# Kernel optimization log

Hardware: AMD Instinct MI355X
Metric: run time of the kernel (lower is better)

## Reference

```python
import jax, jax.numpy as jnp
import numpy as np

B, S, D = 2, 1024, 1024
NH, DQK, DH = 8, 64, 128
CAP = 15.0
EPS = 1e-6


def setup_inputs() -> dict:
    key = jax.random.key(0)
    ks = jax.random.split(key, 8)
    s = 0.02
    return {
        "x": jax.random.normal(ks[0], (B, S, D), jnp.float32),
        "Wq": jax.random.normal(ks[1], (D, NH * DQK), jnp.float32) * s,
        "Wk": jax.random.normal(ks[2], (D, NH * DQK), jnp.float32) * s,
        "Wv": jax.random.normal(ks[3], (D, NH * DH), jnp.float32) * s,
        "Wi": jax.random.normal(ks[4], (D, NH), jnp.float32) * s,
        "bi": jnp.zeros((NH,), jnp.float32),
        "Wf": jax.random.normal(ks[5], (D, NH), jnp.float32) * s,
        "bf": jnp.ones((NH,), jnp.float32),
        "Wog": jax.random.normal(ks[6], (D, D), jnp.float32) * s,
        "ln_w": jnp.ones((NH, DH), jnp.float32),
        "ln_b": jnp.zeros((NH, DH), jnp.float32),
        "Wout": jax.random.normal(ks[7], (NH * DH, D), jnp.float32) * s,
    }


def _mlstm_scan(q, k, v, i, f):
    # q,k: [S,B,NH,DQK]; v: [S,B,NH,DH]; i,f: [S,B,NH]
    b, nh, dqk, dh = q.shape[1], q.shape[2], q.shape[3], v.shape[3]
    scale = dqk ** -0.5
    c0 = jnp.zeros((b, nh, dqk, dh), jnp.float32)
    m0 = jnp.zeros((b, nh), jnp.float32)

    def step(carry, inp):
        c, m = carry
        qt, kt, vt, it, ft = inp
        flog = jax.nn.log_sigmoid(ft)
        m_new = jnp.maximum(flog + m, it)
        f_act = jnp.exp(flog + m - m_new)
        i_act = jnp.exp(it - m_new)
        kv = jnp.einsum('bhi,bhj->bhij', kt, vt)
        c_new = f_act[..., None, None] * c + i_act[..., None, None] * kv
        ht = jnp.einsum('bhij,bhi->bhj', c_new, qt * scale)
        return (c_new, m_new), ht

    _, h = jax.lax.scan(step, (c0, m0), (q, k, v, i, f))
    return h  # [S,B,NH,DH]


def reference(x, Wq, Wk, Wv, Wi, bi, Wf, bf, Wog, ln_w, ln_b, Wout):
    b, s, d = x.shape
    nh, dh = ln_w.shape
    dqk = Wq.shape[1] // nh
    # projections -> time-major [S,B,NH,*]
    q = (x @ Wq).reshape(b, s, nh, dqk).transpose(1, 0, 2, 3)
    k = (x @ Wk).reshape(b, s, nh, dqk).transpose(1, 0, 2, 3)
    v = (x @ Wv).reshape(b, s, nh, dh).transpose(1, 0, 2, 3)
    i = (x @ Wi + bi).transpose(1, 0, 2)
    f = (x @ Wf + bf).transpose(1, 0, 2)
    h = _mlstm_scan(q, k, v, i, f)           # [S,B,NH,DH]
    h = h.transpose(1, 2, 0, 3)              # [B,NH,S,DH]
    # per-head layernorm (unbiased=False variance)
    mean = h.mean(-1, keepdims=True)
    var = ((h - mean) ** 2).mean(-1, keepdims=True)
    hn = (h - mean) / jnp.sqrt(var + EPS)
    hn = hn * ln_w[None, :, None, :] + ln_b[None, :, None, :]
    hn = hn.transpose(0, 2, 1, 3).reshape(b, s, nh * dh)  # [B,S,v_dim]
    o = jax.nn.sigmoid(jnp.tanh((x @ Wog) / CAP) * CAP)
    return (hn * o) @ Wout
```

## Files before the change

### kernel.cpp

```cpp
#include <hip/hip_runtime.h>
#include <math.h>

#define NB_B   2
#define NB_S   1024
#define NB_D   1024
#define NB_NH  8
#define NB_DQK 64
#define NB_DH  128
#define NCH    8
#define CL     128

typedef __attribute__((ext_vector_type(8))) short  short8v;
typedef __attribute__((ext_vector_type(4))) float  f32x4;
typedef __attribute__((ext_vector_type(8))) unsigned short ushort8v;
typedef __attribute__((ext_vector_type(4))) unsigned short ushort4v;

__device__ __forceinline__ unsigned short f2bf(float f) {
  unsigned u = __float_as_uint(f);
  unsigned r = (u + 0x7FFFu + ((u >> 16) & 1u)) >> 16;
  return (unsigned short)r;
}
__device__ __forceinline__ float bf2f(unsigned short h) {
  return __uint_as_float(((unsigned)h) << 16);
}

#define GLD_LDS16(g, l) __builtin_amdgcn_global_load_lds( \
    (const __attribute__((address_space(1))) void*)(g),   \
    (__attribute__((address_space(3))) void*)(l), 16, 0, 0)

#define MFMA_BF16(a, b, c) __builtin_amdgcn_mfma_f32_16x16x32_bf16((a), (b), (c), 0, 0, 0)

constexpr size_t BF(size_t elems) { return elems / 2; }
constexpr size_t SZ_PQK = 2048ull * 1024;
constexpr size_t SZ_PVX = BF(2048ull * 2048);
constexpr size_t SZ_XH  = BF(2048ull * 1024);
constexpr size_t SZ_XL  = BF(2048ull * 1024);
constexpr size_t SZ_WHI = BF(3072ull * 1024);
constexpr size_t SZ_WLO = BF(1024ull * 1024);
constexpr size_t SZ_WTO = BF(1024ull * 1024);
constexpr size_t SZ_GBUF= 16ull * 1024;
constexpr size_t SZ_DL  = 16ull * 8 * 8192;
constexpr size_t SZ_CB  = 16ull * 8 * 8192;
constexpr size_t SZ_HNG = BF(2048ull * 1024);

constexpr size_t OFF_PQK = 0;
constexpr size_t OFF_PVX = OFF_PQK + SZ_PQK;
constexpr size_t OFF_XH  = OFF_PVX + SZ_PVX;
constexpr size_t OFF_XL  = OFF_XH  + SZ_XH;
constexpr size_t OFF_WHI = OFF_XL  + SZ_XL;
constexpr size_t OFF_WLO = OFF_WHI + SZ_WHI;
constexpr size_t OFF_WTO = OFF_WLO + SZ_WLO;
constexpr size_t OFF_IV  = OFF_WTO + SZ_WTO;
constexpr size_t OFF_FV  = OFF_IV  + SZ_GBUF;
constexpr size_t OFF_G   = OFF_FV  + SZ_GBUF;
constexpr size_t OFF_GM  = OFF_G   + SZ_GBUF;
constexpr size_t OFF_DL  = OFF_GM  + SZ_GBUF;
constexpr size_t OFF_CB  = OFF_DL  + SZ_DL;
constexpr size_t OFF_HNG = OFF_CB  + SZ_CB;
constexpr size_t WS_TOTAL = OFF_HNG + SZ_HNG;
static_assert(OFF_XH == OFF_PVX + 2097152, "Pvx is 2048x2048 bf16 = 2,097,152 float slots");

__global__ __launch_bounds__(64) void row_pre(
    const float* __restrict__ x,
    const float* __restrict__ Wi, const float* __restrict__ bi,
    const float* __restrict__ Wf, const float* __restrict__ bf,
    unsigned short* __restrict__ xh, unsigned short* __restrict__ xl,
    float* __restrict__ iv, float* __restrict__ fv)
{
  const int row = blockIdx.x, l = threadIdx.x;
  const float4* xr4 = (const float4*)(x + (size_t)row * NB_D);
  float ai[8] = {}, af[8] = {};
  #pragma unroll
  for (int p = 0; p < 4; ++p) {
    int q4i = l + p * 64;
    float4 xv = xr4[q4i];
    int k0 = q4i * 4;
    const float* xs = (const float*)&xv;
    ushort4v h4, l4;
    #pragma unroll
    for (int j = 0; j < 4; ++j) {
      float xsv = xs[j];
      unsigned short hh = f2bf(xsv);
      h4[j] = hh; l4[j] = f2bf(xsv - bf2f(hh));
      const float4* wi4 = (const float4*)(Wi + (size_t)(k0 + j) * 8);
      const float4* wf4 = (const float4*)(Wf + (size_t)(k0 + j) * 8);
      float4 w0 = wi4[0], w1 = wi4[1];
      float4 v0 = wf4[0], v1 = wf4[1];
      ai[0] += xsv*w0.x; ai[1] += xsv*w0.y; ai[2] += xsv*w0.z; ai[3] += xsv*w0.w;
      ai[4] += xsv*w1.x; ai[5] += xsv*w1.y; ai[6] += xsv*w1.z; ai[7] += xsv*w1.w;
      af[0] += xsv*v0.x; af[1] += xsv*v0.y; af[2] += xsv*v0.z; af[3] += xsv*v0.w;
      af[4] += xsv*v1.x; af[5] += xsv*v1.y; af[6] += xsv*v1.z; af[7] += xsv*v1.w;
    }
    *(ushort4v*)(xh + (size_t)row * NB_D + k0) = h4;
    *(ushort4v*)(xl + (size_t)row * NB_D + k0) = l4;
  }
  #pragma unroll
  for (int off = 1; off < 64; off <<= 1) {
    #pragma unroll
    for (int cc = 0; cc < 8; ++cc) {
      ai[cc] += __shfl_xor(ai[cc], off);
      af[cc] += __shfl_xor(af[cc], off);
    }
  }
  if (l == 0) {
    int b = row >> 10, s = row & (NB_S - 1);
    #pragma unroll
    for (int cc = 0; cc < 8; ++cc) {
      iv[(size_t)(b*NB_NH + cc) * NB_S + s] = ai[cc] + bi[cc];
      fv[(size_t)(b*NB_NH + cc) * NB_S + s] = af[cc] + bf[cc];
    }
  }
}

__device__ __forceinline__ void transp_body(
    const float* __restrict__ src,
    unsigned short* __restrict__ hi, unsigned short* __restrict__ lo,
    int N, int nt, int kt, int tid, float (*Ls)[65])
{
  #pragma unroll
  for (int p = 0; p < 16; ++p) {
    int lin = p * 256 + tid;
    int kr = lin >> 6, nc = lin & 63;
    Ls[kr][nc] = src[(size_t)(kt*64 + kr) * N + nt*64 + nc];
  }
  __syncthreads();
  #pragma unroll
  for (int p = 0; p < 16; ++p) {
    int lin = p * 256 + tid;
    int nr = lin >> 6, kc = lin & 63;
    float v = Ls[kc][nr];
    unsigned short h = f2bf(v);
    size_t di = (size_t)(nt*64 + nr) * 1024 + kt*64 + kc;
    hi[di] = h;
    if (lo) lo[di] = f2bf(v - bf2f(h));
  }
}

__global__ __launch_bounds__(256) void transp5(
    const float* __restrict__ Wq, const float* __restrict__ Wk,
    const float* __restrict__ Wv, const float* __restrict__ Wog,
    const float* __restrict__ Wout,
    unsigned short* __restrict__ Whi, unsigned short* __restrict__ Wlo,
    unsigned short* __restrict__ WtO)
{
  __shared__ float Ls[64][65];
  const int x = blockIdx.x, kt = blockIdx.y, tid = threadIdx.x;
  if (x < 8)       transp_body(Wq,   Whi,              Wlo,            512,  x,      kt, tid, Ls);
  else if (x < 16) transp_body(Wk,   Whi +  512*1024,  Wlo + 512*1024, 512,  x - 8,  kt, tid, Ls);
  else if (x < 32) transp_body(Wv,   Whi + 1024*1024,  nullptr,        1024, x - 16, kt, tid, Ls);
  else if (x < 48) transp_body(Wog,  Whi + 2048*1024,  nullptr,        1024, x - 32, kt, tid, Ls);
  else             transp_body(Wout, WtO,              nullptr,        1024, x - 48, kt, tid, Ls);
}

__global__ __launch_bounds__(256) void gemm_proj(
    const unsigned short* __restrict__ xh,
    const unsigned short* __restrict__ xl,
    const unsigned short* __restrict__ Whi,
    const unsigned short* __restrict__ Wlo,
    float* __restrict__ Pqk, unsigned short* __restrict__ Pvx)
{
  __shared__ __align__(16) char smem[49152];
  const int tid  = threadIdx.x;
  const int bid  = ((blockIdx.x & 7) << 6) | (blockIdx.x >> 3);
  const int wid  = tid >> 6, lane = tid & 63;
  const int wm   = wid >> 1, wn = wid & 1;
  const int lrow = lane & 15;
  const int lk   = (lane >> 4) * 16;
  const int srow = tid >> 3;
  const int scb  = (tid & 7) << 4;
  const int ldsW = wid * 1024;

  if (!(bid & 1)) {
    const int h  = bid >> 1;
    const int ct = h & 7, bm = h >> 3;
    char* Ah = smem;
    char* Al = smem + 8192;
    char* Bh = smem + 16384;
    char* Bl = smem + 32768;
    const char* xhB = (const char*)xh;
    const char* xlB = (const char*)xl;
    const char* whB = (const char*)(Whi + (size_t)ct*128*1024);
    const char* wlB = (const char*)(Wlo + (size_t)ct*128*1024);

    size_t gA[2], gB[4];
    #pragma unroll
    for (int i = 0; i < 2; ++i) {
      int row = i * 32 + srow;
      int cbs = scb ^ ((row & 7) << 4);
      gA[i] = (size_t)(bm*64 + row) * 2048 + cbs;
    }
    #pragma unroll
    for (int i = 0; i < 4; ++i) {
      int row = i * 32 + srow;
      int cbs = scb ^ ((row & 7) << 4);
      gB[i] = (size_t)row * 2048 + cbs;
    }

    f32x4 acc[2][4];
    const f32x4 z4 = { 0.f, 0.f, 0.f, 0.f };
    #pragma unroll
    for (int m = 0; m < 2; ++m)
      #pragma unroll
      for (int n = 0; n < 4; ++n) acc[m][n] = z4;

    for (int kt = 0; kt < 16; ++kt) {
      __syncthreads();
      #pragma unroll
      for (int i = 0; i < 2; ++i) GLD_LDS16(xhB + gA[i] + kt*128, Ah + i*4096 + ldsW);
      #pragma unroll
      for (int i = 0; i < 2; ++i) GLD_LDS16(xlB + gA[i] + kt*128, Al + i*4096 + ldsW);
      #pragma unroll
      for (int i = 0; i < 4; ++i) GLD_LDS16(whB + gB[i] + kt*128, Bh + i*4096 + ldsW);
      #pragma unroll
      for (int i = 0; i < 4; ++i) GLD_LDS16(wlB + gB[i] + kt*128, Bl + i*4096 + ldsW);
      __syncthreads();

      #pragma unroll
      for (int kk = 0; kk < 2; ++kk) {
        short8v ah[2], al[2], bh[4], bl[4];
        #pragma unroll
        for (int m = 0; m < 2; ++m) {
          int row = wm*32 + m*16 + lrow;
          int kb  = (kk*64 + lk) ^ ((row & 7) << 4);
          ah[m] = *(const short8v*)(Ah + row*128 + kb);
          al[m] = *(const short8v*)(Al + row*128 + kb);
        }
        #pragma unroll
        for (int n = 0; n < 4; ++n) {
          int row = wn*64 + n*16 + lrow;
          int kb  = (kk*64 + lk) ^ ((row & 7) << 4);
          bh[n] = *(const short8v*)(Bh + row*128 + kb);
          bl[n] = *(const short8v*)(Bl + row*128 + kb);
        }
        #pragma unroll
        for (int m = 0; m < 2; ++m)
          #pragma unroll
          for (int n = 0; n < 4; ++n) {
            acc[m][n] = MFMA_BF16(ah[m], bh[n], acc[m][n]);
            acc[m][n] = MFMA_BF16(al[m], bh[n], acc[m][n]);
            acc[m][n] = MFMA_BF16(ah[m], bl[n], acc[m][n]);
          }
      }
    }

    const int crow0 = bm*64 + wm*32 + ((lane >> 4) << 2);
    const int ccol0 = ct*128 + wn*64 + lrow;
    #pragma unroll
    for (int m = 0; m < 2; ++m)
      #pragma unroll
      for (int n = 0; n < 4; ++n)
        #pragma unroll
        for (int r = 0; r < 4; ++r)
          Pqk[(size_t)(crow0 + m*16 + r) * 1024 + ccol0 + n*16] = acc[m][n][r];
  } else {
    const int l  = bid >> 1;
    const int ct = l & 15, bm = l >> 4;
    char* As = smem;
    char* Bs = smem + 16384;
    const char* xhB = (const char*)xh;
    const char* wB  = (const char*)(Whi + (size_t)(8 + ct)*128*1024);

    size_t gA[4], gB[4];
    #pragma unroll
    for (int i = 0; i < 4; ++i) {
      int row = i * 32 + srow;
      int cbs = scb ^ ((row & 7) << 4);
      gA[i] = (size_t)(bm*128 + row) * 2048 + cbs;
      gB[i] = (size_t)row * 2048 + cbs;
    }

    f32x4 acc[4][4];
    const f32x4 z4 = { 0.f, 0.f, 0.f, 0.f };
    #pragma unroll
    for (int m = 0; m < 4; ++m)
      #pragma unroll
      for (int n = 0; n < 4; ++n) acc[m][n] = z4;

    for (int kt = 0; kt < 16; ++kt) {
      __syncthreads();
      #pragma unroll
      for (int i = 0; i < 4; ++i) GLD_LDS16(xhB + gA[i] + kt*128, As + i*4096 + ldsW);
      #pragma unroll
      for (int i = 0; i < 4; ++i) GLD_LDS16(wB  + gB[i] + kt*128, Bs + i*4096 + ldsW);
      __syncthreads();

      #pragma unroll
      for (int kk = 0; kk < 2; ++kk) {
        short8v a[4], b[4];
        #pragma unroll
        for (int m = 0; m < 4; ++m) {
          int row = wm*64 + m*16 + lrow;
          int kb  = (kk*64 + lk) ^ ((row & 7) << 4);
          a[m] = *(const short8v*)(As + row*128 + kb);
        }
        #pragma unroll
        for (int n = 0; n < 4; ++n) {
          int row = wn*64 + n*16 + lrow;
          int kb  = (kk*64 + lk) ^ ((row & 7) << 4);
          b[n] = *(const short8v*)(Bs + row*128 + kb);
        }
        #pragma unroll
        for (int m = 0; m < 4; ++m)
          #pragma unroll
          for (int n = 0; n < 4; ++n)
            acc[m][n] = MFMA_BF16(a[m], b[n], acc[m][n]);
      }
    }

    const int crow0 = bm*128 + wm*64 + ((lane >> 4) << 2);
    const int ccol0 = ct*128 + wn*64 + lrow;
    #pragma unroll
    for (int m = 0; m < 4; ++m)
      #pragma unroll
      for (int n = 0; n < 4; ++n)
        #pragma unroll
        for (int r = 0; r < 4; ++r)
          Pvx[(size_t)(crow0 + m*16 + r) * 2048 + ccol0 + n*16] = f2bf(acc[m][n][r]);
  }
}

__global__ __launch_bounds__(256) void gemm_out64(
    const unsigned short* __restrict__ A,
    const unsigned short* __restrict__ Bt,
    float* __restrict__ C, int ldc)
{
  __shared__ __align__(16) unsigned short As[128*64];
  __shared__ __align__(16) unsigned short Bs[64*64];
  const int tid  = threadIdx.x;
  const int bid  = ((blockIdx.x & 7) << 5) | (blockIdx.x >> 3);
  const int cn   = bid & 15, bm = bid >> 4;
  const int wid  = tid >> 6, lane = tid & 63;
  const int wm   = wid >> 1, wn = wid & 1;
  const int lrow = lane & 15;
  const int lk   = (lane >> 4) * 16;

  f32x4 acc[4][2];
  const f32x4 z4 = { 0.f, 0.f, 0.f, 0.f };
  #pragma unroll
  for (int m = 0; m < 4; ++m)
    #pragma unroll
    for (int n = 0; n < 2; ++n) acc[m][n] = z4;

  const int srow = tid >> 3;
  const int scb  = (tid & 7) << 4;
  const char* Ab = (const char*)A;
  const char* Bb = (const char*)Bt;
  size_t gA[4], gB[2];
  #pragma unroll
  for (int i = 0; i < 4; ++i) {
    int row = i * 32 + srow;
    int cbs = scb ^ ((row & 7) << 4);
    gA[i] = (size_t)(bm*128 + row) * 2048 + cbs;
  }
  #pragma unroll
  for (int i = 0; i < 2; ++i) {
    int row = i * 32 + srow;
    int cbs = scb ^ ((row & 7) << 4);
    gB[i] = (size_t)(cn*64 + row) * 2048 + cbs;
  }
  const int ldsW = wid * 1024;

  for (int kt = 0; kt < 16; ++kt) {
    __syncthreads();
    #pragma unroll
    for (int i = 0; i < 4; ++i)
      GLD_LDS16(Ab + gA[i] + kt*128, (char*)As + i*4096 + ldsW);
    #pragma unroll
    for (int i = 0; i < 2; ++i)
      GLD_LDS16(Bb + gB[i] + kt*128, (char*)Bs + i*4096 + ldsW);
    __syncthreads();

    #pragma unroll
    for (int kk = 0; kk < 2; ++kk) {
      short8v a[4], b[2];
      #pragma unroll
      for (int m = 0; m < 4; ++m) {
        int row = wm*64 + m*16 + lrow;
        int kb  = (kk*64 + lk) ^ ((row & 7) << 4);
        a[m] = *(const short8v*)((const char*)As + row*128 + kb);
      }
      #pragma unroll
      for (int n = 0; n < 2; ++n) {
        int row = wn*32 + n*16 + lrow;
        int kb  = (kk*64 + lk) ^ ((row & 7) << 4);
        b[n] = *(const short8v*)((const char*)Bs + row*128 + kb);
      }
      #pragma unroll
      for (int m = 0; m < 4; ++m)
        #pragma unroll
        for (int n = 0; n < 2; ++n)
          acc[m][n] = MFMA_BF16(a[m], b[n], acc[m][n]);
    }
  }

  const int crow0 = bm*128 + wm*64 + ((lane >> 4) << 2);
  const int ccol0 = cn*64 + wn*32 + (lane & 15);
  #pragma unroll
  for (int m = 0; m < 4; ++m)
    #pragma unroll
    for (int n = 0; n < 2; ++n)
      #pragma unroll
      for (int r = 0; r < 4; ++r)
        C[(size_t)(crow0 + m*16 + r) * ldc + ccol0 + n*16] = acc[m][n][r];
}

__global__ __launch_bounds__(64) void gate_scan(
    const float* __restrict__ iv, const float* __restrict__ fv,
    float* __restrict__ gv, float* __restrict__ Gv)
{
  const int bh = blockIdx.x, l = threadIdx.x;
  const int base = bh * NB_S + l * 16;
  float fl[16];
  float run = 0.f;
  #pragma unroll
  for (int u = 0; u < 16; ++u) {
    float fr = fv[base + u];
    float flog = (fr >= 0.f) ? -log1pf(expf(-fr)) : (fr - log1pf(expf(fr)));
    run += flog; fl[u] = run;
  }
  float tot = run, sc = tot;
  #pragma unroll
  for (int off = 1; off < 64; off <<= 1) {
    float t = __shfl_up(sc, off);
    if (l >= off) sc += t;
  }
  float excl = sc - tot;
  float gm[16]; float rmax = -1e30f;
  #pragma unroll
  for (int u = 0; u < 16; ++u) {
    float bt = excl + fl[u];
    float g = iv[base + u] - bt;
    gv[base + u] = g;
    rmax = fmaxf(rmax, g); gm[u] = rmax;
  }
  float mx = rmax;
  #pragma unroll
  for (int off = 1; off < 64; off <<= 1) {
    float t = __shfl_up(mx, off);
    if (l >= off) mx = fmaxf(mx, t);
  }
  float em = __shfl_up(mx, 1);
  if (l == 0) em = -1e30f;
  #pragma unroll
  for (int u = 0; u < 16; ++u)
    Gv[base + u] = fmaxf(0.f, fmaxf(em, gm[u]));
}

__global__ __launch_bounds__(128) void chunk_local(
    const float* __restrict__ Pqk, const unsigned short* __restrict__ Pvx,
    const float* __restrict__ gv, const float* __restrict__ Gv,
    float* __restrict__ Dloc)
{
  __shared__ float ks[16][68];
  __shared__ float vs[16][132];
  __shared__ float wsg[16];
  const int bx = blockIdx.x, bh = bx >> 3, c = bx & 7;
  const int b = bh >> 3, h = bh & 7;
  const int tid = threadIdx.x;
  const int rg = tid >> 3, cg = tid & 7;
  const int i0 = rg * 4;
  float acc[4][16] = {};
  const float Gend = Gv[bh*NB_S + c*CL + CL - 1];
  const float* kbp = Pqk + ((size_t)b*NB_S + c*CL) * 1024 + 512 + h*NB_DQK;
  const unsigned short* vbp = Pvx + ((size_t)b*NB_S + c*CL) * 2048 + h*NB_DH;
  const float* gbp = gv + bh*NB_S + c*CL;
  for (int sb = 0; sb < 8; ++sb) {
    __syncthreads();
    #pragma unroll
    for (int p = 0; p < 2; ++p) {
      int qd = tid + p*128; int r = qd >> 4, cq = qd & 15;
      *(float4*)(&ks[r][cq*4]) = *(const float4*)(kbp + (size_t)(sb*16 + r)*1024 + cq*4);
    }
    #pragma unroll
    for (int p = 0; p < 4; ++p) {
      int qd = tid + p*128; int r = qd >> 5, cq = qd & 31;
      ushort4v v4 = *(const ushort4v*)(vbp + (size_t)(sb*16 + r)*2048 + cq*4);
      vs[r][cq*4+0] = bf2f(v4[0]); vs[r][cq*4+1] = bf2f(v4[1]);
      vs[r][cq*4+2] = bf2f(v4[2]); vs[r][cq*4+3] = bf2f(v4[3]);
    }
    if (tid < 16) wsg[tid] = expf(gbp[sb*16 + tid] - Gend);
    __syncthreads();
    #pragma unroll
    for (int s = 0; s < 16; ++s) {
      float w = wsg[s];
      float4 kq = *(const float4*)(&ks[s][i0]);
      float wk[4] = { w*kq.x, w*kq.y, w*kq.z, w*kq.w };
      #pragma unroll
      for (int m = 0; m < 4; ++m) {
        float4 vq = *(const float4*)(&vs[s][cg*4 + m*32]);
        #pragma unroll
        for (int u = 0; u < 4; ++u) {
          acc[u][m*4+0] += wk[u]*vq.x;
          acc[u][m*4+1] += wk[u]*vq.y;
          acc[u][m*4+2] += wk[u]*vq.z;
          acc[u][m*4+3] += wk[u]*vq.w;
        }
      }
    }
  }
  float* dst = Dloc + ((size_t)bh*NCH + c) * (NB_DQK*NB_DH);
  #pragma unroll
  for (int u = 0; u < 4; ++u)
    #pragma unroll
    for (int m = 0; m < 4; ++m) {
      float4 o4 = { acc[u][m*4+0], acc[u][m*4+1], acc[u][m*4+2], acc[u][m*4+3] };
      *(float4*)(dst + (size_t)(i0+u)*NB_DH + cg*4 + m*32) = o4;
    }
}

__global__ __launch_bounds__(256) void chunk_combine(
    const float* __restrict__ Dloc, const float* __restrict__ Gv,
    float* __restrict__ Cbef)
{
  const int bh = blockIdx.x >> 3, sl = blockIdx.x & 7;
  const int fo = sl*1024 + threadIdx.x*4;
  float4 acc = { 0.f, 0.f, 0.f, 0.f };
  float Gprev = 0.f;
  for (int c = 0; c < NCH; ++c) {
    const float* dl = Dloc + ((size_t)bh*NCH + c)*8192 + fo;
    float* cb = Cbef + ((size_t)bh*NCH + c)*8192 + fo;
    float Gend = Gv[bh*NB_S + c*CL + CL - 1];
    float decay = (c == 0) ? 0.f : expf(Gprev - Gend);
    *(float4*)cb = acc;
    float4 d = *(const float4*)dl;
    acc.x = acc.x*decay + d.x;
    acc.y = acc.y*decay + d.y;
    acc.z = acc.z*decay + d.z;
    acc.w = acc.w*decay + d.w;
    Gprev = Gend;
  }
}

__global__ __launch_bounds__(256,1) void chunk_out(
    const float* __restrict__ Pqk, const unsigned short* __restrict__ Pvx,
    const float* __restrict__ gv, const float* __restrict__ Gv,
    const float* __restrict__ Cbef,
    const float* __restrict__ lnw, const float* __restrict__ lnb,
    unsigned short* __restrict__ hng)
{
  __shared__ __align__(16) char smem[131072];
  __shared__ float gsh[128], Gsh[128], rsh[128];
  constexpr int QH = 0, QL = 8192, KH = 16384, KL = 32768;
  constexpr int ATT = 49152, VT = 65536, CBH = 98304, CBL = 114688;

  const int bx = ((blockIdx.x & 7) << 5) | (blockIdx.x >> 3);
  const int half = bx & 1, c = (bx >> 1) & 7, bh = bx >> 4;
  const int b = bh >> 3, h = bh & 7;
  const int tid = threadIdx.x;
  const int wid = tid >> 6, lane = tid & 63;
  const int lrow = lane & 15;
  const int lkB  = (lane >> 4) * 16;
  const size_t rowbase = (size_t)b*NB_S + (size_t)c*CL;
  const int sgbase = bh*NB_S + c*CL;

  if (tid < 128) {
    float gval = gv[sgbase + tid];
    float Gval = Gv[sgbase + tid];
    gsh[tid] = gval; Gsh[tid] = Gval;
    float Gprev = (c > 0) ? Gv[sgbase - 1] : 0.f;
    rsh[tid] = 0.125f * expf(Gprev - Gval);
  }

  #pragma unroll
  for (int p = 0; p < 4; ++p) {
    int lin = p*256 + tid;
    int row = lin >> 4, i0 = (lin & 15) * 4;
    float4 v4 = *(const float4*)(Pqk + (rowbase + half*64 + row)*1024 + h*NB_DQK + i0);
    float vv[4] = { v4.x, v4.y, v4.z, v4.w };
    ushort4v h4, l4;
    #pragma unroll
    for (int j = 0; j < 4; ++j) {
      unsigned short hh = f2bf(vv[j]); h4[j] = hh; l4[j] = f2bf(vv[j] - bf2f(hh));
    }
    int off = (row*128 + i0*2) ^ ((row & 7) << 4);
    *(ushort4v*)(smem + QH + off) = h4;
    *(ushort4v*)(smem + QL + off) = l4;
  }
  #pragma unroll
  for (int p = 0; p < 8; ++p) {
    int lin = p*256 + tid;
    int row = lin >> 4, i0 = (lin & 15) * 4;
    float4 v4 = *(const float4*)(Pqk + (rowbase + row)*1024 + 512 + h*NB_DQK + i0);
    float vv[4] = { v4.x, v4.y, v4.z, v4.w };
    ushort4v h4, l4;
    #pragma unroll
    for (int j = 0; j < 4; ++j) {
      unsigned short hh = f2bf(vv[j]); h4[j] = hh; l4[j] = f2bf(vv[j] - bf2f(hh));
    }
    int off = (row*128 + i0*2) ^ ((row & 7) << 4);
    *(ushort4v*)(smem + KH + off) = h4;
    *(ushort4v*)(smem + KL + off) = l4;
  }
  #pragma unroll
  for (int p = 0; p < 8; ++p) {
    int lin = p*256 + tid;
    int s = lin >> 4, j0 = (lin & 15) * 8;
    ushort8v v8 = *(const ushort8v*)(Pvx + (rowbase + s)*2048 + h*NB_DH + j0);
    #pragma unroll
    for (int j = 0; j < 8; ++j) {
      int jj = j0 + j;
      int off = (jj*256 + s*2) ^ ((jj & 7) << 4);
      *(unsigned short*)(smem + VT + off) = v8[j];
    }
  }
  {
    const float* Cbp = Cbef + ((size_t)bh*NCH + c)*(NB_DQK*NB_DH);
    #pragma unroll
    for (int p = 0; p < 8; ++p) {
      int lin = p*256 + tid;
      int i = lin >> 5, j0 = (lin & 31) * 4;
      float4 v4 = *(const float4*)(Cbp + (size_t)i*NB_DH + j0);
      float vv[4] = { v4.x, v4.y, v4.z, v4.w };
      #pragma unroll
      for (int w = 0; w < 4; ++w) {
        int jj = j0 + w;
        int off = (jj*128 + i*2) ^ ((jj & 7) << 4);
        unsigned short hh = f2bf(vv[w]);
        *(unsigned short*)(smem + CBH + off) = hh;
        *(unsigned short*)(smem + CBL + off) = f2bf(vv[w] - bf2f(hh));
      }
    }
  }
  __syncthreads();

  const f32x4 z4 = { 0.f, 0.f, 0.f, 0.f };
  const int trow = wid*16 + lrow;

  f32x4 sacc[8];
  #pragma unroll
  for (int n = 0; n < 8; ++n) sacc[n] = z4;
  #pragma unroll
  for (int kk = 0; kk < 2; ++kk) {
    int qb = kk*64 + lkB;
    int ab = (trow*128 + qb) ^ ((trow & 7) << 4);
    short8v aqh = *(const short8v*)(smem + QH + ab);
    short8v aql = *(const short8v*)(smem + QL + ab);
    #pragma unroll
    for (int n = 0; n < 8; ++n) {
      int srw = n*16 + lrow;
      int bb = (srw*128 + qb) ^ ((srw & 7) << 4);
      short8v bkh = *(const short8v*)(smem + KH + bb);
      short8v bkl = *(const short8v*)(smem + KL + bb);
      sacc[n] = MFMA_BF16(aqh, bkh, sacc[n]);
      sacc[n] = MFMA_BF16(aql, bkh, sacc[n]);
      sacc[n] = MFMA_BF16(aqh, bkl, sacc[n]);
    }
  }
  {
    int td[4]; float gt[4];
    #pragma unroll
    for (int r = 0; r < 4; ++r) {
      td[r] = wid*16 + ((lane >> 4) << 2) + r;
      gt[r] = Gsh[half*64 + td[r]];
    }
    #pragma unroll
    for (int n = 0; n < 8; ++n) {
      int s = n*16 + lrow;
      float gs = gsh[s];
      #pragma unroll
      for (int r = 0; r < 4; ++r) {
        float w = 0.125f * expf(gs - gt[r]);
        float val = (s <= half*64 + td[r]) ? sacc[n][r]*w : 0.f;
        int off = (td[r]*256 + s*2) ^ ((td[r] & 7) << 4);
        *(unsigned short*)(smem + ATT + off) = f2bf(val);
      }
    }
  }

  f32x4 h2[8];
  #pragma unroll
  for (int n = 0; n < 8; ++n) h2[n] = z4;
  #pragma unroll
  for (int kk = 0; kk < 2; ++kk) {
    int qb = kk*64 + lkB;
    int ab = (trow*128 + qb) ^ ((trow & 7) << 4);
    short8v aqh = *(const short8v*)(smem + QH + ab);
    short8v aql = *(const short8v*)(smem + QL + ab);
    #pragma unroll
    for (int n = 0; n < 8; ++n) {
      int jrw = n*16 + lrow;
      int bb = (jrw*128 + qb) ^ ((jrw & 7) << 4);
      short8v bch = *(const short8v*)(smem + CBH + bb);
      short8v bcl = *(const short8v*)(smem + CBL + bb);
      h2[n] = MFMA_BF16(aqh, bch, h2[n]);
      h2[n] = MFMA_BF16(aql, bch, h2[n]);
      h2[n] = MFMA_BF16(aqh, bcl, h2[n]);
    }
  }
  __syncthreads();

  f32x4 h1[8];
  #pragma unroll
  for (int n = 0; n < 8; ++n) h1[n] = z4;
  #pragma unroll
  for (int kk = 0; kk < 4; ++kk) {
    int ab = (trow*256 + kk*64 + lkB) ^ ((trow & 7) << 4);
    short8v aat = *(const short8v*)(smem + ATT + ab);
    #pragma unroll
    for (int n = 0; n < 8; ++n) {
      int jrw = n*16 + lrow;
      int bb = (jrw*256 + kk*64 + lkB) ^ ((jrw & 7) << 4);
      short8v bvt = *(const short8v*)(smem + VT + bb);
      h1[n] = MFMA_BF16(aat, bvt, h1[n]);
    }
  }
  __syncthreads();

  float* Hb = (float*)smem;
  {
    #pragma unroll
    for (int r = 0; r < 4; ++r) {
      int tl = wid*16 + ((lane >> 4) << 2) + r;
      float rr = rsh[half*64 + tl];
      #pragma unroll
      for (int n = 0; n < 8; ++n)
        Hb[tl*132 + n*16 + lrow] = h1[n][r] + rr*h2[n][r];
    }
  }
  __syncthreads();

  const int tr = tid >> 4, tc = tid & 15;
  float lw[8], lb[8];
  {
    float4 a0 = *(const float4*)(lnw + h*NB_DH + tc*4);
    float4 a1 = *(const float4*)(lnw + h*NB_DH + tc*4 + 64);
    lw[0]=a0.x; lw[1]=a0.y; lw[2]=a0.z; lw[3]=a0.w;
    lw[4]=a1.x; lw[5]=a1.y; lw[6]=a1.z; lw[7]=a1.w;
    float4 b0 = *(const float4*)(lnb + h*NB_DH + tc*4);
    float4 b1 = *(const float4*)(lnb + h*NB_DH + tc*4 + 64);
    lb[0]=b0.x; lb[1]=b0.y; lb[2]=b0.z; lb[3]=b0.w;
    lb[4]=b1.x; lb[5]=b1.y; lb[6]=b1.z; lb[7]=b1.w;
  }
  #pragma unroll
  for (int u = 0; u < 4; ++u) {
    int tl = tr*4 + u;
    int t  = half*64 + tl;
    float hrow[8];
    float4 hl0 = *(const float4*)(&Hb[tl*132 + tc*4]);
    float4 hl1 = *(const float4*)(&Hb[tl*132 + tc*4 + 64]);
    hrow[0]=hl0.x; hrow[1]=hl0.y; hrow[2]=hl0.z; hrow[3]=hl0.w;
    hrow[4]=hl1.x; hrow[5]=hl1.y; hrow[6]=hl1.z; hrow[7]=hl1.w;
    float sum = 0.f, ssq = 0.f;
    #pragma unroll
    for (int x = 0; x < 8; ++x) { sum += hrow[x]; ssq += hrow[x]*hrow[x]; }
    #pragma unroll
    for (int off = 1; off < 16; off <<= 1) {
      sum += __shfl_xor(sum, off);
      ssq += __shfl_xor(ssq, off);
    }
    float mean = sum * (1.f/NB_DH);
    float var  = ssq * (1.f/NB_DH) - mean*mean;
    float rstd = rsqrtf(var + 1e-6f);
    #pragma unroll
    for (int m = 0; m < 2; ++m) {
      ushort4v xo4 = *(const ushort4v*)(Pvx + (rowbase + t)*2048 + 1024 + h*NB_DH + tc*4 + m*64);
      float xov[4] = { bf2f(xo4[0]), bf2f(xo4[1]), bf2f(xo4[2]), bf2f(xo4[3]) };
      unsigned short res[4];
      #pragma unroll
      for (int w = 0; w < 4; ++w) {
        int x = m*4 + w;
        float hn = (hrow[x] - mean)*rstd*lw[x] + lb[x];
        float tt = tanhf(xov[w]*(1.f/15.f))*15.f;
        float o = 1.f/(1.f + expf(-tt));
        res[w] = f2bf(hn*o);
      }
      ushort4v r4 = { res[0], res[1], res[2], res[3] };
      *(ushort4v*)(hng + (rowbase + t)*1024 + h*NB_DH + tc*4 + m*64) = r4;
    }
  }
}

extern "C" void kernel_launch(void* const* d_in, const int* in_sizes, int n_in,
                              void* d_out, int out_size, void* d_ws, size_t ws_size,
                              hipStream_t stream)
{
  (void)in_sizes; (void)n_in; (void)out_size; (void)ws_size;
  const float* x   = (const float*)d_in[0];
  const float* Wq  = (const float*)d_in[1];
  const float* Wk  = (const float*)d_in[2];
  const float* Wv  = (const float*)d_in[3];
  const float* Wi  = (const float*)d_in[4];
  const float* bi  = (const float*)d_in[5];
  const float* Wf  = (const float*)d_in[6];
  const float* bf  = (const float*)d_in[7];
  const float* Wog = (const float*)d_in[8];
  const float* lnw = (const float*)d_in[9];
  const float* lnb = (const float*)d_in[10];
  const float* Wout= (const float*)d_in[11];
  float* out = (float*)d_out;
  float* ws  = (float*)d_ws;

  float*          Pqk = ws + OFF_PQK;
  unsigned short* Pvx = (unsigned short*)(ws + OFF_PVX);
  unsigned short* xh  = (unsigned short*)(ws + OFF_XH);
  unsigned short* xl  = (unsigned short*)(ws + OFF_XL);
  unsigned short* Whi = (unsigned short*)(ws + OFF_WHI);
  unsigned short* Wlo = (unsigned short*)(ws + OFF_WLO);
  unsigned short* WtO = (unsigned short*)(ws + OFF_WTO);
  float*          iv  = ws + OFF_IV;
  float*          fv  = ws + OFF_FV;
  float*          g   = ws + OFF_G;
  float*          G   = ws + OFF_GM;
  float*          Dl  = ws + OFF_DL;
  float*          Cb  = ws + OFF_CB;
  unsigned short* hng = (unsigned short*)(ws + OFF_HNG);

  row_pre <<<2048, 64, 0, stream>>>(x, Wi, bi, Wf, bf, xh, xl, iv, fv);
  transp5 <<<dim3(64,16), 256, 0, stream>>>(Wq, Wk, Wv, Wog, Wout, Whi, Wlo, WtO);
  gate_scan<<<16, 64, 0, stream>>>(iv, fv, g, G);

  gemm_proj<<<512, 256, 0, stream>>>(xh, xl, Whi, Wlo, Pqk, Pvx);

  chunk_local  <<<128, 128, 0, stream>>>(Pqk, Pvx, g, G, Dl);
  chunk_combine<<<128, 256, 0, stream>>>(Dl, G, Cb);
  chunk_out    <<<256, 256, 0, stream>>>(Pqk, Pvx, g, G, Cb, lnw, lnb, hng);

  gemm_out64<<<256, 256, 0, stream>>>(hng, WtO, out, 1024);
}
```

Before: 135.1 us.

## Fuse row_pre with weight transpose and fold chunk_combine into chunk_out

Merges the per-row x split/gate projection kernel and the weight transpose kernel into one prep launch, packing 4 rows per 256-thread block. Removes chunk_combine and its Cbef buffer: each chunk_out block now recomputes its inter-chunk state as an exp-weighted sum of all earlier chunks' local states read from Dloc. This saves two launches and one global round trip, but adds redundant reads and FMAs that grow with chunk index (up to 7 chunks of 32KB per block).

Result: faster. 129.6 us (-4.0%).

```diff
diff --git a/kernel.cpp b/kernel.cpp
--- a/kernel.cpp
+++ b/kernel.cpp
@@ -40,7 +40,6 @@
 constexpr size_t SZ_WTO = BF(1024ull * 1024);
 constexpr size_t SZ_GBUF= 16ull * 1024;
 constexpr size_t SZ_DL  = 16ull * 8 * 8192;
-constexpr size_t SZ_CB  = 16ull * 8 * 8192;
 constexpr size_t SZ_HNG = BF(2048ull * 1024);
 
 constexpr size_t OFF_PQK = 0;
@@ -55,62 +54,9 @@
 constexpr size_t OFF_G   = OFF_FV  + SZ_GBUF;
 constexpr size_t OFF_GM  = OFF_G   + SZ_GBUF;
 constexpr size_t OFF_DL  = OFF_GM  + SZ_GBUF;
-constexpr size_t OFF_CB  = OFF_DL  + SZ_DL;
-constexpr size_t OFF_HNG = OFF_CB  + SZ_CB;
+constexpr size_t OFF_HNG = OFF_DL  + SZ_DL;
 constexpr size_t WS_TOTAL = OFF_HNG + SZ_HNG;
 static_assert(OFF_XH == OFF_PVX + 2097152, "Pvx is 2048x2048 bf16 = 2,097,152 float slots");
-
-__global__ __launch_bounds__(64) void row_pre(
-    const float* __restrict__ x,
-    const float* __restrict__ Wi, const float* __restrict__ bi,
-    const float* __restrict__ Wf, const float* __restrict__ bf,
-    unsigned short* __restrict__ xh, unsigned short* __restrict__ xl,
-    float* __restrict__ iv, float* __restrict__ fv)
-{
-  const int row = blockIdx.x, l = threadIdx.x;
-  const float4* xr4 = (const float4*)(x + (size_t)row * NB_D);
-  float ai[8] = {}, af[8] = {};
-  #pragma unroll
-  for (int p = 0; p < 4; ++p) {
-    int q4i = l + p * 64;
-    float4 xv = xr4[q4i];
-    int k0 = q4i * 4;
-    const float* xs = (const float*)&xv;
-    ushort4v h4, l4;
-    #pragma unroll
-    for (int j = 0; j < 4; ++j) {
-      float xsv = xs[j];
-      unsigned short hh = f2bf(xsv);
-      h4[j] = hh; l4[j] = f2bf(xsv - bf2f(hh));
-      const float4* wi4 = (const float4*)(Wi + (size_t)(k0 + j) * 8);
-      const float4* wf4 = (const float4*)(Wf + (size_t)(k0 + j) * 8);
-      float4 w0 = wi4[0], w1 = wi4[1];
-      float4 v0 = wf4[0], v1 = wf4[1];
-      ai[0] += xsv*w0.x; ai[1] += xsv*w0.y; ai[2] += xsv*w0.z; ai[3] += xsv*w0.w;
-      ai[4] += xsv*w1.x; ai[5] += xsv*w1.y; ai[6] += xsv*w1.z; ai[7] += xsv*w1.w;
-      af[0] += xsv*v0.x; af[1] += xsv*v0.y; af[2] += xsv*v0.z; af[3] += xsv*v0.w;
-      af[4] += xsv*v1.x; af[5] += xsv*v1.y; af[6] += xsv*v1.z; af[7] += xsv*v1.w;
-    }
-    *(ushort4v*)(xh + (size_t)row * NB_D + k0) = h4;
-    *(ushort4v*)(xl + (size_t)row * NB_D + k0) = l4;
-  }
-  #pragma unroll
-  for (int off = 1; off < 64; off <<= 1) {
-    #pragma unroll
-    for (int cc = 0; cc < 8; ++cc) {
-      ai[cc] += __shfl_xor(ai[cc], off);
-      af[cc] += __shfl_xor(af[cc], off);
-    }
-  }
-  if (l == 0) {
-    int b = row >> 10, s = row & (NB_S - 1);
-    #pragma unroll
-    for (int cc = 0; cc < 8; ++cc) {
-      iv[(size_t)(b*NB_NH + cc) * NB_S + s] = ai[cc] + bi[cc];
-      fv[(size_t)(b*NB_NH + cc) * NB_S + s] = af[cc] + bf[cc];
-    }
-  }
-}
 
 __device__ __forceinline__ void transp_body(
     const float* __restrict__ src,
@@ -136,20 +82,74 @@
   }
 }
 
-__global__ __launch_bounds__(256) void transp5(
+__global__ __launch_bounds__(256) void prep(
+    const float* __restrict__ x,
+    const float* __restrict__ Wi, const float* __restrict__ bi,
+    const float* __restrict__ Wf, const float* __restrict__ bf,
     const float* __restrict__ Wq, const float* __restrict__ Wk,
     const float* __restrict__ Wv, const float* __restrict__ Wog,
     const float* __restrict__ Wout,
+    unsigned short* __restrict__ xh, unsigned short* __restrict__ xl,
+    float* __restrict__ iv, float* __restrict__ fv,
     unsigned short* __restrict__ Whi, unsigned short* __restrict__ Wlo,
     unsigned short* __restrict__ WtO)
 {
   __shared__ float Ls[64][65];
-  const int x = blockIdx.x, kt = blockIdx.y, tid = threadIdx.x;
-  if (x < 8)       transp_body(Wq,   Whi,              Wlo,            512,  x,      kt, tid, Ls);
-  else if (x < 16) transp_body(Wk,   Whi +  512*1024,  Wlo + 512*1024, 512,  x - 8,  kt, tid, Ls);
-  else if (x < 32) transp_body(Wv,   Whi + 1024*1024,  nullptr,        1024, x - 16, kt, tid, Ls);
-  else if (x < 48) transp_body(Wog,  Whi + 2048*1024,  nullptr,        1024, x - 32, kt, tid, Ls);
-  else             transp_body(Wout, WtO,              nullptr,        1024, x - 48, kt, tid, Ls);
+  const int bx = blockIdx.x, tid = threadIdx.x;
+  if (bx < 512) {
+    const int row = bx * 4 + (tid >> 6);
+    const int l = tid & 63;
+    const float4* xr4 = (const float4*)(x + (size_t)row * NB_D);
+    float ai[8] = {}, af[8] = {};
+    #pragma unroll
+    for (int p = 0; p < 4; ++p) {
+      int q4i = l + p * 64;
+      float4 xv = xr4[q4i];
+      int k0 = q4i * 4;
+      const float* xs = (const float*)&xv;
+      ushort4v h4, l4;
+      #pragma unroll
+      for (int j = 0; j < 4; ++j) {
+        float xsv = xs[j];
+        unsigned short hh = f2bf(xsv);
+        h4[j] = hh; l4[j] = f2bf(xsv - bf2f(hh));
+        const float4* wi4 = (const float4*)(Wi + (size_t)(k0 + j) * 8);
+        const float4* wf4 = (const float4*)(Wf + (size_t)(k0 + j) * 8);
+        float4 w0 = wi4[0], w1 = wi4[1];
+        float4 v0 = wf4[0], v1 = wf4[1];
+        ai[0] += xsv*w0.x; ai[1] += xsv*w0.y; ai[2] += xsv*w0.z; ai[3] += xsv*w0.w;
+        ai[4] += xsv*w1.x; ai[5] += xsv*w1.y; ai[6] += xsv*w1.z; ai[7] += xsv*w1.w;
+        af[0] += xsv*v0.x; af[1] += xsv*v0.y; af[2] += xsv*v0.z; af[3] += xsv*v0.w;
+        af[4] += xsv*v1.x; af[5] += xsv*v1.y; af[6] += xsv*v1.z; af[7] += xsv*v1.w;
+      }
+      *(ushort4v*)(xh + (size_t)row * NB_D + k0) = h4;
+      *(ushort4v*)(xl + (size_t)row * NB_D + k0) = l4;
+    }
+    #pragma unroll
+    for (int off = 1; off < 64; off <<= 1) {
+      #pragma unroll
+      for (int cc = 0; cc < 8; ++cc) {
+        ai[cc] += __shfl_xor(ai[cc], off);
+        af[cc] += __shfl_xor(af[cc], off);
+      }
+    }
+    if (l == 0) {
+      int b = row >> 10, s = row & (NB_S - 1);
+      #pragma unroll
+      for (int cc = 0; cc < 8; ++cc) {
+        iv[(size_t)(b*NB_NH + cc) * NB_S + s] = ai[cc] + bi[cc];
+        fv[(size_t)(b*NB_NH + cc) * NB_S + s] = af[cc] + bf[cc];
+      }
+    }
+  } else {
+    const int idx = bx - 512;
+    const int xq = idx & 63, kt = idx >> 6;
+    if (xq < 8)       transp_body(Wq,   Whi,              Wlo,            512,  xq,      kt, tid, Ls);
+    else if (xq < 16) transp_body(Wk,   Whi +  512*1024,  Wlo + 512*1024, 512,  xq - 8,  kt, tid, Ls);
+    else if (xq < 32) transp_body(Wv,   Whi + 1024*1024,  nullptr,        1024, xq - 16, kt, tid, Ls);
+    else if (xq < 48) transp_body(Wog,  Whi + 2048*1024,  nullptr,        1024, xq - 32, kt, tid, Ls);
+    else              transp_body(Wout, WtO,              nullptr,        1024, xq - 48, kt, tid, Ls);
+  }
 }
 
 __global__ __launch_bounds__(256) void gemm_proj(
@@ -508,33 +508,10 @@
     }
 }
 
-__global__ __launch_bounds__(256) void chunk_combine(
-    const float* __restrict__ Dloc, const float* __restrict__ Gv,
-    float* __restrict__ Cbef)
-{
-  const int bh = blockIdx.x >> 3, sl = blockIdx.x & 7;
-  const int fo = sl*1024 + threadIdx.x*4;
-  float4 acc = { 0.f, 0.f, 0.f, 0.f };
-  float Gprev = 0.f;
-  for (int c = 0; c < NCH; ++c) {
-    const float* dl = Dloc + ((size_t)bh*NCH + c)*8192 + fo;
-    float* cb = Cbef + ((size_t)bh*NCH + c)*8192 + fo;
-    float Gend = Gv[bh*NB_S + c*CL + CL - 1];
-    float decay = (c == 0) ? 0.f : expf(Gprev - Gend);
-    *(float4*)cb = acc;
-    float4 d = *(const float4*)dl;
-    acc.x = acc.x*decay + d.x;
-    acc.y = acc.y*decay + d.y;
-    acc.z = acc.z*decay + d.z;
-    acc.w = acc.w*decay + d.w;
-    Gprev = Gend;
-  }
-}
-
 __global__ __launch_bounds__(256,1) void chunk_out(
     const float* __restrict__ Pqk, const unsigned short* __restrict__ Pvx,
     const float* __restrict__ gv, const float* __restrict__ Gv,
-    const float* __restrict__ Cbef,
+    const float* __restrict__ Dloc,
     const float* __restrict__ lnw, const float* __restrict__ lnb,
     unsigned short* __restrict__ hng)
 {
@@ -604,13 +581,25 @@
     }
   }
   {
-    const float* Cbp = Cbef + ((size_t)bh*NCH + c)*(NB_DQK*NB_DH);
+    float4 cbacc[8];
+    #pragma unroll
+    for (int p = 0; p < 8; ++p) cbacc[p] = float4{0.f,0.f,0.f,0.f};
+    const float Gcm1 = (c > 0) ? Gv[sgbase - 1] : 0.f;
+    for (int cp = 0; cp < c; ++cp) {
+      float wgt = expf(Gv[bh*NB_S + cp*CL + CL - 1] - Gcm1);
+      const float4* dl4 = (const float4*)(Dloc + ((size_t)bh*NCH + cp)*8192);
+      #pragma unroll
+      for (int p = 0; p < 8; ++p) {
+        float4 d = dl4[p*256 + tid];
+        cbacc[p].x += wgt*d.x; cbacc[p].y += wgt*d.y;
+        cbacc[p].z += wgt*d.z; cbacc[p].w += wgt*d.w;
+      }
+    }
     #pragma unroll
     for (int p = 0; p < 8; ++p) {
       int lin = p*256 + tid;
       int i = lin >> 5, j0 = (lin & 31) * 4;
-      float4 v4 = *(const float4*)(Cbp + (size_t)i*NB_DH + j0);
-      float vv[4] = { v4.x, v4.y, v4.z, v4.w };
+      float vv[4] = { cbacc[p].x, cbacc[p].y, cbacc[p].z, cbacc[p].w };
       #pragma unroll
       for (int w = 0; w < 4; ++w) {
         int jj = j0 + w;
@@ -802,18 +791,16 @@
   float*          g   = ws + OFF_G;
   float*          G   = ws + OFF_GM;
   float*          Dl  = ws + OFF_DL;
-  float*          Cb  = ws + OFF_CB;
   unsigned short* hng = (unsigned short*)(ws + OFF_HNG);
 
-  row_pre <<<2048, 64, 0, stream>>>(x, Wi, bi, Wf, bf, xh, xl, iv, fv);
-  transp5 <<<dim3(64,16), 256, 0, stream>>>(Wq, Wk, Wv, Wog, Wout, Whi, Wlo, WtO);
+  prep     <<<1536, 256, 0, stream>>>(x, Wi, bi, Wf, bf, Wq, Wk, Wv, Wog, Wout,
+                                      xh, xl, iv, fv, Whi, Wlo, WtO);
   gate_scan<<<16, 64, 0, stream>>>(iv, fv, g, G);
 
   gemm_proj<<<512, 256, 0, stream>>>(xh, xl, Whi, Wlo, Pqk, Pvx);
 
-  chunk_local  <<<128, 128, 0, stream>>>(Pqk, Pvx, g, G, Dl);
-  chunk_combine<<<128, 256, 0, stream>>>(Dl, G, Cb);
-  chunk_out    <<<256, 256, 0, stream>>>(Pqk, Pvx, g, G, Cb, lnw, lnb, hng);
-
-  gemm_out64<<<256, 256, 0, stream>>>(hng, WtO, out, 1024);
-}
+  chunk_local<<<128, 128, 0, stream>>>(Pqk, Pvx, g, G, Dl);
+  chunk_out  <<<256, 256, 0, stream>>>(Pqk, Pvx, g, G, Dl, lnw, lnb, hng);
+
+  gemm_out64 <<<256, 256, 0, stream>>>(hng, WtO, out, 1024);
+}
```
